# Optimization experiments

Hardware: AMD Instinct MI355X
Metric: run time of the kernel (lower is better)

Reference implementation:

```python
import jax, jax.numpy as jnp
import numpy as np

N_RAYS = 8192
M = 524288
GX, GY, GZ = 160, 160, 128
NFEAT = 12
POS_PE, VIEW_PE = 10, 4
WIDTH = 128
POS_DIM = 3 + 3 * POS_PE * 2      # 63
VIEW_DIM = 3 + 3 * VIEW_PE * 2    # 27
DIM0 = NFEAT + POS_DIM            # 75
ACT_SHIFT = float(np.log(1.0 / (1.0 - 1e-6) - 1.0))  # density bias shift from alpha_init
INTERVAL = 0.5                    # stepsize * voxel_size_ratio
XYZ_MIN, XYZ_MAX = -1.0, 1.0


def posemb(x, n_pe):
    # x: [N,3] -> [N, 3 + 3*n_pe*2], matching cat([x, sin(x*freq), cos(x*freq)])
    freq = 2.0 ** jnp.arange(n_pe, dtype=x.dtype)
    xf = (x[..., None] * freq).reshape(x.shape[0], -1)
    return jnp.concatenate([x, jnp.sin(xf), jnp.cos(xf)], axis=-1)


def trilinear(grid, xyz):
    # grid: [X,Y,Z,C]; xyz: [M,3] in world coords. align_corners=True bilinear (grid_sample).
    sz_f = jnp.array(grid.shape[:3], jnp.float32)
    sz_i = jnp.array(grid.shape[:3], jnp.int32)
    t = (xyz - XYZ_MIN) / (XYZ_MAX - XYZ_MIN) * (sz_f - 1.0)
    t = jnp.clip(t, 0.0, sz_f - 1.0)
    i0 = jnp.clip(jnp.floor(t).astype(jnp.int32), 0, sz_i - 2)
    f = t - i0.astype(t.dtype)
    out = jnp.zeros((xyz.shape[0], grid.shape[-1]), t.dtype)
    for dx in (0, 1):
        for dy in (0, 1):
            for dz in (0, 1):
                w = ((f[:, 0] if dx else 1.0 - f[:, 0])
                     * (f[:, 1] if dy else 1.0 - f[:, 1])
                     * (f[:, 2] if dz else 1.0 - f[:, 2]))
                out = out + w[:, None] * grid[i0[:, 0] + dx, i0[:, 1] + dy, i0[:, 2] + dz]
    return out


def mask_lookup(mask, xyz):
    # nearest-neighbor maskcache_lookup: ijk = round(xyz*scale + shift)
    sz_f = jnp.array(mask.shape, jnp.float32)
    scale = (sz_f - 1.0) / (XYZ_MAX - XYZ_MIN)
    shift = -XYZ_MIN * scale
    ijk = jnp.clip(jnp.round(xyz * scale + shift).astype(jnp.int32), 0,
                   jnp.array(mask.shape, jnp.int32) - 1)
    return mask[ijk[:, 0], ijk[:, 1], ijk[:, 2]]


def alphas2weights(alpha, ray_id, n_rays):
    # segmented T_i = prod_{j<i in ray}(1-alpha_j); weights = T*alpha (ray_id sorted)
    log1a = jnp.log(jnp.clip(1.0 - alpha, 1e-10, 1.0))
    excl = jnp.cumsum(log1a) - log1a                      # global exclusive cumsum
    seg_tot = jax.ops.segment_sum(log1a, ray_id, num_segments=n_rays)
    seg_start = jnp.cumsum(seg_tot) - seg_tot             # exclusive prefix over rays
    T = jnp.exp(excl - seg_start[ray_id])
    weights = T * alpha
    alphainv_last = jnp.exp(seg_tot)
    return weights, alphainv_last


def setup_inputs() -> dict:
    key = jax.random.key(0)
    ks = jax.random.split(key, 16)
    xyz = jax.random.uniform(ks[0], (M, 3), jnp.float32) * (XYZ_MAX - XYZ_MIN) + XYZ_MIN
    ray_id = jnp.sort(jax.random.randint(ks[1], (M,), 0, N_RAYS))
    viewdirs = jax.random.normal(ks[2], (N_RAYS, 3), jnp.float32)
    viewdirs = viewdirs / jnp.linalg.norm(viewdirs, axis=-1, keepdims=True)
    mask = jax.random.uniform(ks[3], (GX, GY, GZ)) > 0.1
    density = jax.random.normal(ks[4], (GX, GY, GZ), jnp.float32) * 0.5
    k0 = jax.random.normal(ks[5], (GX, GY, GZ, NFEAT), jnp.float32) * 0.1
    s = 0.05
    W0 = jax.random.normal(ks[6], (DIM0, WIDTH), jnp.float32) * s
    b0 = jnp.zeros((WIDTH,), jnp.float32)
    W1 = jax.random.normal(ks[7], (WIDTH, WIDTH), jnp.float32) * s
    b1 = jnp.zeros((WIDTH,), jnp.float32)
    W2 = jax.random.normal(ks[8], (WIDTH, WIDTH), jnp.float32) * s
    b2 = jnp.zeros((WIDTH,), jnp.float32)
    Wr = jax.random.normal(ks[9], (WIDTH + VIEW_DIM, 3), jnp.float32) * s
    br = jnp.zeros((3,), jnp.float32)
    return {"xyz": xyz, "ray_id": ray_id, "viewdirs": viewdirs, "mask": mask,
            "density": density, "k0": k0, "W0": W0, "b0": b0, "W1": W1, "b1": b1,
            "W2": W2, "b2": b2, "Wr": Wr, "br": br}


def reference(xyz, ray_id, viewdirs, mask, density, k0, W0, b0, W1, b1, W2, b2, Wr, br):
    # 1) empty-space skipping via mask cache (kept as multiplicative mask for static shapes)
    m = mask_lookup(mask, xyz).astype(xyz.dtype)
    # 2) trilinear density query + raw2alpha
    d = trilinear(density[..., None], xyz)[:, 0]
    alpha = 1.0 - (1.0 + jnp.exp(d + ACT_SHIFT)) ** (-INTERVAL)
    alpha = alpha * m
    # 3) segmented alpha compositing (Alphas2Weights)
    weights, alphainv_last = alphas2weights(alpha, ray_id, N_RAYS)
    # 4) feature query + view MLP -> rgb
    feat = trilinear(k0, xyz)                              # [M, NFEAT]
    h = jnp.concatenate([feat, posemb(xyz, POS_PE)], -1)   # [M, DIM0]
    h = jax.nn.relu(h @ W0 + b0)
    h = jax.nn.relu(h @ W1 + b1)
    h = jax.nn.relu(h @ W2 + b2)
    ve = posemb(viewdirs, VIEW_PE)[ray_id]                 # [M, VIEW_DIM]
    rgb = jax.nn.sigmoid(jnp.concatenate([h, ve], -1) @ Wr + br)
    # 5) composite per ray + white background
    rgb_marched = jax.ops.segment_sum(weights[:, None] * rgb, ray_id, num_segments=N_RAYS)
    rgb_marched = rgb_marched + alphainv_last[:, None] * 1.0
    return rgb_marched
```

## Files before the change

### kernel.cpp

```cpp
#include <hip/hip_runtime.h>
#include <hip/hip_bf16.h>

#define M_SAMPLES 524288
#define NRAYS 8192
#define GXD 160
#define GYD 160
#define GZD 128
#define GYZ (GYD*GZD)
#define NVOX (GXD*GYD*GZD)
#define ACT_SHIFT -13.81550955796f
#define ROWA 136
#define ROWB 136
#define SAMP 64

typedef __bf16 bf16x8 __attribute__((ext_vector_type(8)));
typedef float f32x4 __attribute__((ext_vector_type(4)));
typedef float f32x16 __attribute__((ext_vector_type(16)));
typedef float f32v2 __attribute__((ext_vector_type(2)));

static __device__ inline unsigned short f2bf(float f){
  __hip_bfloat16 h = __float2bfloat16(f);
  unsigned short u; __builtin_memcpy(&u, &h, 2); return u;
}
static __device__ inline float flo(unsigned int u){ return __uint_as_float(u << 16); }
static __device__ inline float fhi(unsigned int u){ return __uint_as_float(u & 0xffff0000u); }

#if defined(__has_builtin)
#if __has_builtin(__builtin_amdgcn_cvt_pk_bf16_f32)
#define HAVE_PK_BF16 1
#endif
#if __has_builtin(__builtin_amdgcn_cvt_pk_f32_fp8) && __has_builtin(__builtin_amdgcn_cvt_pk_fp8_f32)
#define HAVE_FP8 1
#endif
#endif

static __device__ inline unsigned int packbf(float a, float b){
#ifdef HAVE_PK_BF16
  typedef __bf16 bf16v2 __attribute__((ext_vector_type(2)));
  bf16v2 r = __builtin_amdgcn_cvt_pk_bf16_f32(a, b);
  unsigned int u; __builtin_memcpy(&u, &r, 4); return u;
#else
  return (unsigned int)f2bf(a) | ((unsigned int)f2bf(b) << 16);
#endif
}

struct Tri {
  int ix, iy, iz;
  float wx0, wx1, wy0, wy1, wz0, wz1;
};
static __device__ inline Tri tri_setup(float x, float y, float z){
  Tri t;
  float tx = (x+1.f)*0.5f*(float)(GXD-1); tx = fminf(fmaxf(tx,0.f),(float)(GXD-1));
  float ty = (y+1.f)*0.5f*(float)(GYD-1); ty = fminf(fmaxf(ty,0.f),(float)(GYD-1));
  float tz = (z+1.f)*0.5f*(float)(GZD-1); tz = fminf(fmaxf(tz,0.f),(float)(GZD-1));
  t.ix = min((int)tx, GXD-2); t.iy = min((int)ty, GYD-2); t.iz = min((int)tz, GZD-2);
  float fx = tx-t.ix, fy = ty-t.iy, fz = tz-t.iz;
  t.wx0 = 1.f-fx; t.wx1 = fx; t.wy0 = 1.f-fy; t.wy1 = fy; t.wz0 = 1.f-fz; t.wz1 = fz;
  return t;
}

#define NB_REPACK (NVOX/256)
#define NB_W      184
#define NB_RT     (NRAYS/256)
__global__ __launch_bounds__(256) void k_prep(
    const float* __restrict__ density, const float* __restrict__ k0,
    uint4* __restrict__ packed,
    const unsigned int* __restrict__ mw, int* __restrict__ flag,
    const float* __restrict__ W0, const float* __restrict__ W1,
    const float* __restrict__ W2, const float* __restrict__ Wr,
    const float* __restrict__ br,
    unsigned short* __restrict__ wt0, unsigned short* __restrict__ wt1,
    unsigned short* __restrict__ wt2, unsigned short* __restrict__ wtr,
    const float* __restrict__ vd, float* __restrict__ rayterm3)
{
  int b = blockIdx.x;
  if(b < NB_REPACK){
    int v = b*256 + threadIdx.x;
    const float4* kp = (const float4*)(k0 + (size_t)v*12);
    float4 a = kp[0], bb = kp[1], c = kp[2];
#ifdef HAVE_FP8
    uint4 o;
    o.x = __float_as_uint(density[v]);
    int w;
    w = __builtin_amdgcn_cvt_pk_fp8_f32(a.x, a.y, 0, false);
    w = __builtin_amdgcn_cvt_pk_fp8_f32(a.z, a.w, w, true);
    o.y = (unsigned int)w;
    w = __builtin_amdgcn_cvt_pk_fp8_f32(bb.x, bb.y, 0, false);
    w = __builtin_amdgcn_cvt_pk_fp8_f32(bb.z, bb.w, w, true);
    o.z = (unsigned int)w;
    w = __builtin_amdgcn_cvt_pk_fp8_f32(c.x, c.y, 0, false);
    w = __builtin_amdgcn_cvt_pk_fp8_f32(c.z, c.w, w, true);
    o.w = (unsigned int)w;
    packed[v] = o;
#else
    uint4 o0, o1;
    o0.x = __float_as_uint(density[v]);
    o0.y = packbf(a.x, a.y); o0.z = packbf(a.z, a.w); o0.w = packbf(bb.x, bb.y);
    o1.x = packbf(bb.z, bb.w); o1.y = packbf(c.x, c.y); o1.z = packbf(c.z, c.w);
    o1.w = 0;
    packed[(size_t)v*2]   = o0;
    packed[(size_t)v*2+1] = o1;
#endif
    return;
  }
  if(b == NB_REPACK){
    unsigned int v = mw[threadIdx.x & 63];
    unsigned long long any = __ballot(v > 1u);
    if(threadIdx.x == 0) *flag = (any != 0ull) ? 1 : 0;
    return;
  }
  if(b < NB_REPACK + 1 + NB_W){
    int t = (b - NB_REPACK - 1)*256 + threadIdx.x;
    if(t < 128*96){
      int n = t/96, k = t%96;
      wt0[t] = f2bf((k < 75) ? W0[k*128 + n] : 0.f);
    } else if(t < 128*96 + 16384){
      int j = t - 128*96; int n = j/128, k = j%128;
      wt1[j] = f2bf(W1[k*128 + n]);
    } else if(t < 128*96 + 32768){
      int j = t - 128*96 - 16384; int n = j/128, k = j%128;
      wt2[j] = f2bf(W2[k*128 + n]);
    } else if(t < 128*96 + 32768 + 16*128){
      int j = t - 128*96 - 32768; int n = j/128, k = j%128;
      wtr[j] = f2bf((n < 3) ? Wr[k*3 + n] : 0.f);
    }
    return;
  }
  int ray = (b - NB_REPACK - 1 - NB_W)*256 + threadIdx.x;
  if(ray >= NRAYS) return;
  float v0 = vd[ray*3+0], v1 = vd[ray*3+1], v2 = vd[ray*3+2];
  float vej[27];
  vej[0] = v0; vej[1] = v1; vej[2] = v2;
  #pragma unroll
  for(int ci = 0; ci < 3; ++ci){
    float xv = (ci == 0) ? v0 : ((ci == 1) ? v1 : v2);
    #pragma unroll
    for(int p = 0; p < 4; ++p){
      float arg = xv * (float)(1 << p);
      vej[3 + ci*4 + p]  = __sinf(arg);
      vej[15 + ci*4 + p] = __cosf(arg);
    }
  }
  float rt0 = br[0], rt1 = br[1], rt2 = br[2];
  #pragma unroll
  for(int j = 0; j < 27; ++j){
    const float* wr = Wr + (128 + j)*3;
    rt0 += vej[j]*wr[0]; rt1 += vej[j]*wr[1]; rt2 += vej[j]*wr[2];
  }
  rayterm3[ray*3+0] = rt0; rayterm3[ray*3+1] = rt1; rayterm3[ray*3+2] = rt2;
}

template<int KDIM, int SROW, int DROW>
static __device__ inline void layer32(const unsigned short* src, unsigned short* dst,
    const unsigned short* __restrict__ wt, const float* __restrict__ bias,
    int tile_n, int ln, int kh)
{
  constexpr int NS = KDIM/16;
  const unsigned short* wbase  = wt + (tile_n*32 + ln)*KDIM + kh*8;
  const unsigned short* abase0 = src + (ln)*SROW + kh*8;
  const unsigned short* abase1 = src + (32 + ln)*SROW + kh*8;
  f32x16 acc0 = {0.f,0.f,0.f,0.f,0.f,0.f,0.f,0.f,0.f,0.f,0.f,0.f,0.f,0.f,0.f,0.f};
  f32x16 acc1 = acc0;
  __builtin_amdgcn_s_setprio(1);
  #pragma unroll
  for(int st = 0; st < NS; ++st){
    bf16x8 wf = *(const bf16x8*)(wbase + st*16);
    bf16x8 a0 = *(const bf16x8*)(abase0 + st*16);
    bf16x8 a1 = *(const bf16x8*)(abase1 + st*16);
    acc0 = __builtin_amdgcn_mfma_f32_32x32x16_bf16(wf, a0, acc0, 0, 0, 0);
    acc1 = __builtin_amdgcn_mfma_f32_32x32x16_bf16(wf, a1, acc1, 0, 0, 0);
  }
  __builtin_amdgcn_s_setprio(0);
  #pragma unroll
  for(int rep = 0; rep < 2; ++rep){
    const f32x16& acc = rep ? acc1 : acc0;
    int scol = rep*32 + ln;
    #pragma unroll
    for(int g = 0; g < 4; ++g){
      int n0 = tile_n*32 + g*8 + kh*4;
      float4 bv = *(const float4*)(bias + n0);
      unsigned int lo = packbf(fmaxf(acc[4*g+0] + bv.x, 0.f), fmaxf(acc[4*g+1] + bv.y, 0.f));
      unsigned int hi = packbf(fmaxf(acc[4*g+2] + bv.z, 0.f), fmaxf(acc[4*g+3] + bv.w, 0.f));
      unsigned long long o = (unsigned long long)lo | ((unsigned long long)hi << 32);
      *(unsigned long long*)(dst + scol*DROW + n0) = o;
    }
  }
}

template<int PACKED>
__global__ __launch_bounds__(256) void k_mlp(const float* __restrict__ xyz,
    const uint4* __restrict__ packed,
    const float* __restrict__ density, const float* __restrict__ k0,
    const void* __restrict__ mask, const int* __restrict__ flag,
    const int* __restrict__ ray_id,
    const unsigned short* __restrict__ wt0, const unsigned short* __restrict__ wt1,
    const unsigned short* __restrict__ wt2, const unsigned short* __restrict__ wtr,
    const float* __restrict__ b0, const float* __restrict__ b1,
    const float* __restrict__ b2,
    const float* __restrict__ rayterm3, float4* __restrict__ rgba_out)
{
  __shared__ alignas(16) unsigned short hA[SAMP*ROWA];
  __shared__ alignas(16) unsigned short hB[SAMP*ROWB];
  __shared__ float red[SAMP][4];
  __shared__ int ray_s[SAMP];

  int tid = threadIdx.x;
  int lane = tid & 63, wave = tid >> 6;
  int blk = blockIdx.x*SAMP;

  {
    int smp = tid >> 2, corner = tid & 3;
    int i = blk + smp;
    float x = xyz[3*i+0], y = xyz[3*i+1], z = xyz[3*i+2];
    Tri t = tri_setup(x, y, z);
    int dx = corner & 1, dy = corner >> 1;
    float wxy = (dx ? t.wx1 : t.wx0) * (dy ? t.wy1 : t.wy0);
    float w0 = wxy*t.wz0, w1 = wxy*t.wz1;
    size_t vox = (size_t)((t.ix+dx)*GYZ + (t.iy+dy)*GZD + t.iz);
    float pd;
    float pf[12];
#ifdef HAVE_FP8
    if(PACKED){
      uint4 q0 = packed[vox], q1 = packed[vox+1];
      pd = w0*__uint_as_float(q0.x) + w1*__uint_as_float(q1.x);
      f32v2 a, b;
      a = __builtin_amdgcn_cvt_pk_f32_fp8((int)q0.y, false);
      b = __builtin_amdgcn_cvt_pk_f32_fp8((int)q1.y, false);
      pf[0] = w0*a.x + w1*b.x;  pf[1] = w0*a.y + w1*b.y;
      a = __builtin_amdgcn_cvt_pk_f32_fp8((int)q0.y, true);
      b = __builtin_amdgcn_cvt_pk_f32_fp8((int)q1.y, true);
      pf[2] = w0*a.x + w1*b.x;  pf[3] = w0*a.y + w1*b.y;
      a = __builtin_amdgcn_cvt_pk_f32_fp8((int)q0.z, false);
      b = __builtin_amdgcn_cvt_pk_f32_fp8((int)q1.z, false);
      pf[4] = w0*a.x + w1*b.x;  pf[5] = w0*a.y + w1*b.y;
      a = __builtin_amdgcn_cvt_pk_f32_fp8((int)q0.z, true);
      b = __builtin_amdgcn_cvt_pk_f32_fp8((int)q1.z, true);
      pf[6] = w0*a.x + w1*b.x;  pf[7] = w0*a.y + w1*b.y;
      a = __builtin_amdgcn_cvt_pk_f32_fp8((int)q0.w, false);
      b = __builtin_amdgcn_cvt_pk_f32_fp8((int)q1.w, false);
      pf[8] = w0*a.x + w1*b.x;  pf[9] = w0*a.y + w1*b.y;
      a = __builtin_amdgcn_cvt_pk_f32_fp8((int)q0.w, true);
      b = __builtin_amdgcn_cvt_pk_f32_fp8((int)q1.w, true);
      pf[10]= w0*a.x + w1*b.x;  pf[11]= w0*a.y + w1*b.y;
    }
#else
    if(PACKED){
      const uint4* pv = packed + vox*2;
      uint4 q0 = pv[0], q1 = pv[1], q2 = pv[2], q3 = pv[3];
      pd = w0*__uint_as_float(q0.x) + w1*__uint_as_float(q2.x);
      pf[0]  = w0*flo(q0.y) + w1*flo(q2.y);  pf[1]  = w0*fhi(q0.y) + w1*fhi(q2.y);
      pf[2]  = w0*flo(q0.z) + w1*flo(q2.z);  pf[3]  = w0*fhi(q0.z) + w1*fhi(q2.z);
      pf[4]  = w0*flo(q0.w) + w1*flo(q2.w);  pf[5]  = w0*fhi(q0.w) + w1*fhi(q2.w);
      pf[6]  = w0*flo(q1.x) + w1*flo(q3.x);  pf[7]  = w0*fhi(q1.x) + w1*fhi(q3.x);
      pf[8]  = w0*flo(q1.y) + w1*flo(q3.y);  pf[9]  = w0*fhi(q1.y) + w1*fhi(q3.y);
      pf[10] = w0*flo(q1.z) + w1*flo(q3.z);  pf[11] = w0*fhi(q1.z) + w1*fhi(q3.z);
    }
#endif
    if(!PACKED){
      pd = w0*density[vox] + w1*density[vox+1];
      const float4* v = (const float4*)(k0 + vox*12);
      float4 a0 = v[0], a1 = v[1], a2 = v[2];
      float4 c0 = v[3], c1 = v[4], c2 = v[5];
      pf[0] = w0*a0.x + w1*c0.x;  pf[1] = w0*a0.y + w1*c0.y;
      pf[2] = w0*a0.z + w1*c0.z;  pf[3] = w0*a0.w + w1*c0.w;
      pf[4] = w0*a1.x + w1*c1.x;  pf[5] = w0*a1.y + w1*c1.y;
      pf[6] = w0*a1.z + w1*c1.z;  pf[7] = w0*a1.w + w1*c1.w;
      pf[8] = w0*a2.x + w1*c2.x;  pf[9] = w0*a2.y + w1*c2.y;
      pf[10]= w0*a2.z + w1*c2.z;  pf[11]= w0*a2.w + w1*c2.w;
    }
    #pragma unroll
    for(int m2 = 1; m2 < 4; m2 <<= 1){
      pd += __shfl_xor(pd, m2);
      #pragma unroll
      for(int j = 0; j < 12; ++j) pf[j] += __shfl_xor(pf[j], m2);
    }
    if(corner == 0){
      int mx = (int)rintf(x*79.5f + 79.5f); mx = min(max(mx,0), GXD-1);
      int my = (int)rintf(y*79.5f + 79.5f); my = min(max(my,0), GYD-1);
      int mz = (int)rintf(z*63.5f + 63.5f); mz = min(max(mz,0), GZD-1);
      int midx = mx*GYZ + my*GZD + mz;
      bool mm = (*flag) ? (((const unsigned char*)mask)[midx] != 0)
                        : (((const int*)mask)[midx] != 0);
      float e = __expf(pd + ACT_SHIFT);
      float alpha = 1.f - rsqrtf(1.f + e);
      if(!mm) alpha = 0.f;
      red[smp][3] = alpha;
      unsigned int d[8];
      #pragma unroll
      for(int j = 0; j < 6; ++j) d[j] = packbf(pf[2*j], pf[2*j+1]);
      d[6] = packbf(x, y);
      d[7] = packbf(z, __sinf(x));
      uint4* p = (uint4*)(hA + smp*ROWA);
      p[0] = make_uint4(d[0],d[1],d[2],d[3]);
      p[1] = make_uint4(d[4],d[5],d[6],d[7]);
    } else if(corner == 1){
      uint4* p = (uint4*)(hA + smp*ROWA + 80);
      p[0] = make_uint4(0,0,0,0);
      p[1] = make_uint4(0,0,0,0);
      ray_s[smp] = ray_id[i];
    }
  }

  {
    int smp = tid & 63, chunk = 1 + (tid >> 6);
    int i2 = blk + smp;
    float x = xyz[3*i2+0], y = xyz[3*i2+1], z = xyz[3*i2+2];
    float vv[16];
    #pragma unroll
    for(int j = 0; j < 16; ++j){
      int c = chunk*16 + j;
      float r;
      if(c >= 75) r = 0.f;
      else {
        int q = (c < 45) ? (c-15) : (c-45);
        int ci = q/10, p = q - ci*10;
        float xv = (ci == 0) ? x : ((ci == 1) ? y : z);
        float a = xv * (float)(1 << p);
        r = (c < 45) ? __sinf(a) : __cosf(a);
      }
      vv[j] = r;
    }
    unsigned int d[8];
    #pragma unroll
    for(int j = 0; j < 8; ++j) d[j] = packbf(vv[2*j], vv[2*j+1]);
    uint4* p = (uint4*)(hA + smp*ROWA + chunk*16);
    p[0] = make_uint4(d[0],d[1],d[2],d[3]);
    p[1] = make_uint4(d[4],d[5],d[6],d[7]);
  }
  __syncthreads();

  int ln = lane & 31, kh = lane >> 5;
  layer32< 96, ROWA, ROWB>(hA, hB, wt0, b0, wave, ln, kh);  __syncthreads();
  layer32<128, ROWB, ROWA>(hB, hA, wt1, b1, wave, ln, kh);  __syncthreads();
  layer32<128, ROWA, ROWB>(hA, hB, wt2, b2, wave, ln, kh);  __syncthreads();

  {
    int col = lane & 15, q = lane >> 4;
    int mt = wave;
    f32x4 acc = {0.f, 0.f, 0.f, 0.f};
    const unsigned short* arow = hB + (mt*16 + col)*ROWB + q*8;
    const unsigned short* wrow = wtr + col*128 + q*8;
    __builtin_amdgcn_s_setprio(1);
    #pragma unroll
    for(int ks = 0; ks < 4; ++ks){
      bf16x8 af = *(const bf16x8*)(arow + ks*32);
      bf16x8 bfr = *(const bf16x8*)(wrow + ks*32);
      acc = __builtin_amdgcn_mfma_f32_16x16x32_bf16(af, bfr, acc, 0, 0, 0);
    }
    __builtin_amdgcn_s_setprio(0);
    if(col < 3){
      #pragma unroll
      for(int r = 0; r < 4; ++r){
        int sl = mt*16 + q*4 + r;
        float v = acc[r] + rayterm3[ray_s[sl]*3 + col];
        red[sl][col] = __fdividef(1.f, 1.f + __expf(-v));
      }
    }
  }
  __syncthreads();

  if(tid < SAMP){
    rgba_out[blk + tid] = make_float4(red[tid][0], red[tid][1], red[tid][2], red[tid][3]);
  }
}

__global__ __launch_bounds__(256) void k_comp2(const int* __restrict__ ray_id,
    const float4* __restrict__ rgba, float* __restrict__ out)
{
  int r = blockIdx.x*4 + (threadIdx.x >> 6);
  int lane = threadIdx.x & 63;
  int lo = 0, hi = M_SAMPLES;
  while(lo < hi){ int mid = (lo+hi) >> 1; if(ray_id[mid] < r) lo = mid+1; else hi = mid; }
  int s = lo;
  int lo2 = s, hi2 = M_SAMPLES;
  while(lo2 < hi2){ int mid = (lo2+hi2) >> 1; if(ray_id[mid] < r+1) lo2 = mid+1; else hi2 = mid; }
  int e = lo2;

  float carry = 1.f;
  float ar = 0.f, ag = 0.f, ab = 0.f;
  for(int base = s; base < e; base += 64){
    int idx = base + lane;
    float4 c = (idx < e) ? rgba[idx] : make_float4(0.f,0.f,0.f,0.f);
    float a = c.w;
    float incl = 1.f - a;
    #pragma unroll
    for(int d2 = 1; d2 < 64; d2 <<= 1){
      float t = __shfl_up(incl, d2);
      if(lane >= d2) incl *= t;
    }
    float excl = __shfl_up(incl, 1);
    if(lane == 0) excl = 1.f;
    float w = carry * excl * a;
    ar += w*c.x; ag += w*c.y; ab += w*c.z;
    carry *= __shfl(incl, 63);
  }
  #pragma unroll
  for(int m2 = 1; m2 < 64; m2 <<= 1){
    ar += __shfl_xor(ar, m2);
    ag += __shfl_xor(ag, m2);
    ab += __shfl_xor(ab, m2);
  }
  if(lane == 0){
    out[3*r+0] = ar + carry;
    out[3*r+1] = ag + carry;
    out[3*r+2] = ab + carry;
  }
}

extern "C" void kernel_launch(void* const* d_in, const int* in_sizes, int n_in,
                              void* d_out, int out_size, void* d_ws, size_t ws_size,
                              hipStream_t stream)
{
  const float* xyz      = (const float*)d_in[0];
  const int*   ray_id   = (const int*)  d_in[1];
  const float* viewdirs = (const float*)d_in[2];
  const void*  mask     =               d_in[3];
  const float* density  = (const float*)d_in[4];
  const float* k0       = (const float*)d_in[5];
  const float* W0 = (const float*)d_in[6];  const float* b0 = (const float*)d_in[7];
  const float* W1 = (const float*)d_in[8];  const float* b1 = (const float*)d_in[9];
  const float* W2 = (const float*)d_in[10]; const float* b2 = (const float*)d_in[11];
  const float* Wr = (const float*)d_in[12]; const float* br = (const float*)d_in[13];
  float* out = (float*)d_out;

  char* ws = (char*)d_ws;
  size_t off = 0;
  auto take = [&](size_t nbytes) -> void* {
    void* p = ws + off;
    off = (off + nbytes + 255) & ~(size_t)255;
    return p;
  };
  int*            flag     = (int*)           take(4);
  unsigned short* wt0      = (unsigned short*)take(128*96*2);
  unsigned short* wt1      = (unsigned short*)take(128*128*2);
  unsigned short* wt2      = (unsigned short*)take(128*128*2);
  unsigned short* wtr      = (unsigned short*)take(16*128*2);
  float*          rayterm3 = (float*)         take((size_t)NRAYS*3*4);
  float4*         rgba_ws  = (float4*)        take((size_t)M_SAMPLES*16);
#ifdef HAVE_FP8
  uint4*          packed   = (uint4*)         take((size_t)NVOX*16);
#else
  uint4*          packed   = (uint4*)         take((size_t)NVOX*32);
#endif
  bool use_packed = (ws_size >= off);

  k_prep<<<NB_REPACK + 1 + NB_W + NB_RT, 256, 0, stream>>>(
      density, k0, packed, (const unsigned int*)mask, flag,
      W0, W1, W2, Wr, br, wt0, wt1, wt2, wtr, viewdirs, rayterm3);
  if(use_packed){
    k_mlp<1><<<M_SAMPLES/SAMP, 256, 0, stream>>>(xyz, packed, density, k0, mask, flag,
                                                 ray_id, wt0, wt1, wt2, wtr,
                                                 b0, b1, b2, rayterm3, rgba_ws);
  } else {
    k_mlp<0><<<M_SAMPLES/SAMP, 256, 0, stream>>>(xyz, packed, density, k0, mask, flag,
                                                 ray_id, wt0, wt1, wt2, wtr,
                                                 b0, b1, b2, rayterm3, rgba_ws);
  }
  k_comp2<<<NRAYS/4, 256, 0, stream>>>(ray_id, rgba_ws, out);
}
```

Measured before the change: 422.2 us.

## Prefetch next-layer MLP weights into registers during current layer epilogue

Splits the per-layer MFMA routine into compute, weight-load and epilogue parts so each layer's global weight fragments are loaded into registers before they are needed. The first layer's weights load before the trilinear gather, and later weights and the head weights are fetched while the previous layer's epilogue runs. Launch bounds also gain a minimum-blocks hint of 4. This hides global weight-load latency behind other work, at the cost of more live registers and possible spills under the occupancy constraint.

Result: no change. 417.1 us (-1.2%).

```diff
diff --git a/kernel.cpp b/kernel.cpp
--- a/kernel.cpp
+++ b/kernel.cpp
@@ -150,27 +150,39 @@
   rayterm3[ray*3+0] = rt0; rayterm3[ray*3+1] = rt1; rayterm3[ray*3+2] = rt2;
 }
 
-template<int KDIM, int SROW, int DROW>
-static __device__ inline void layer32(const unsigned short* src, unsigned short* dst,
-    const unsigned short* __restrict__ wt, const float* __restrict__ bias,
-    int tile_n, int ln, int kh)
+template<int KDIM, int SROW>
+static __device__ __forceinline__ void mfma_layer(const unsigned short* src,
+    const bf16x8* wf, f32x16& acc0, f32x16& acc1, int ln, int kh)
 {
   constexpr int NS = KDIM/16;
-  const unsigned short* wbase  = wt + (tile_n*32 + ln)*KDIM + kh*8;
   const unsigned short* abase0 = src + (ln)*SROW + kh*8;
   const unsigned short* abase1 = src + (32 + ln)*SROW + kh*8;
-  f32x16 acc0 = {0.f,0.f,0.f,0.f,0.f,0.f,0.f,0.f,0.f,0.f,0.f,0.f,0.f,0.f,0.f,0.f};
-  f32x16 acc1 = acc0;
+  f32x16 z = {0.f,0.f,0.f,0.f,0.f,0.f,0.f,0.f,0.f,0.f,0.f,0.f,0.f,0.f,0.f,0.f};
+  acc0 = z; acc1 = z;
   __builtin_amdgcn_s_setprio(1);
   #pragma unroll
   for(int st = 0; st < NS; ++st){
-    bf16x8 wf = *(const bf16x8*)(wbase + st*16);
     bf16x8 a0 = *(const bf16x8*)(abase0 + st*16);
     bf16x8 a1 = *(const bf16x8*)(abase1 + st*16);
-    acc0 = __builtin_amdgcn_mfma_f32_32x32x16_bf16(wf, a0, acc0, 0, 0, 0);
-    acc1 = __builtin_amdgcn_mfma_f32_32x32x16_bf16(wf, a1, acc1, 0, 0, 0);
+    acc0 = __builtin_amdgcn_mfma_f32_32x32x16_bf16(wf[st], a0, acc0, 0, 0, 0);
+    acc1 = __builtin_amdgcn_mfma_f32_32x32x16_bf16(wf[st], a1, acc1, 0, 0, 0);
   }
   __builtin_amdgcn_s_setprio(0);
+}
+
+template<int NS>
+static __device__ __forceinline__ void load_wf(const unsigned short* wbase, bf16x8* wf){
+  #pragma unroll
+  for(int st = 0; st < NS; ++st) wf[st] = *(const bf16x8*)(wbase + st*16);
+}
+
+template<int DROW>
+static __device__ __forceinline__ void epilogue(const f32x16& acc0, const f32x16& acc1,
+    unsigned short* dst, const float* __restrict__ bias, int tile_n, int ln, int kh)
+{
+  float4 bv[4];
+  #pragma unroll
+  for(int g = 0; g < 4; ++g) bv[g] = *(const float4*)(bias + tile_n*32 + g*8 + kh*4);
   #pragma unroll
   for(int rep = 0; rep < 2; ++rep){
     const f32x16& acc = rep ? acc1 : acc0;
@@ -178,9 +190,8 @@
     #pragma unroll
     for(int g = 0; g < 4; ++g){
       int n0 = tile_n*32 + g*8 + kh*4;
-      float4 bv = *(const float4*)(bias + n0);
-      unsigned int lo = packbf(fmaxf(acc[4*g+0] + bv.x, 0.f), fmaxf(acc[4*g+1] + bv.y, 0.f));
-      unsigned int hi = packbf(fmaxf(acc[4*g+2] + bv.z, 0.f), fmaxf(acc[4*g+3] + bv.w, 0.f));
+      unsigned int lo = packbf(fmaxf(acc[4*g+0] + bv[g].x, 0.f), fmaxf(acc[4*g+1] + bv[g].y, 0.f));
+      unsigned int hi = packbf(fmaxf(acc[4*g+2] + bv[g].z, 0.f), fmaxf(acc[4*g+3] + bv[g].w, 0.f));
       unsigned long long o = (unsigned long long)lo | ((unsigned long long)hi << 32);
       *(unsigned long long*)(dst + scol*DROW + n0) = o;
     }
@@ -188,7 +199,7 @@
 }
 
 template<int PACKED>
-__global__ __launch_bounds__(256) void k_mlp(const float* __restrict__ xyz,
+__global__ __launch_bounds__(256, 4) void k_mlp(const float* __restrict__ xyz,
     const uint4* __restrict__ packed,
     const float* __restrict__ density, const float* __restrict__ k0,
     const void* __restrict__ mask, const int* __restrict__ flag,
@@ -207,6 +218,10 @@
   int tid = threadIdx.x;
   int lane = tid & 63, wave = tid >> 6;
   int blk = blockIdx.x*SAMP;
+  int ln = lane & 31, kh = lane >> 5;
+
+  bf16x8 wf[8];
+  load_wf<6>(wt0 + (wave*32 + ln)*96 + kh*8, wf);
 
   {
     int smp = tid >> 2, corner = tid & 3;
@@ -329,29 +344,44 @@
   }
   __syncthreads();
 
-  int ln = lane & 31, kh = lane >> 5;
-  layer32< 96, ROWA, ROWB>(hA, hB, wt0, b0, wave, ln, kh);  __syncthreads();
-  layer32<128, ROWB, ROWA>(hB, hA, wt1, b1, wave, ln, kh);  __syncthreads();
-  layer32<128, ROWA, ROWB>(hA, hB, wt2, b2, wave, ln, kh);  __syncthreads();
-
+  f32x16 acc0, acc1;
+
+  mfma_layer<96, ROWA>(hA, wf, acc0, acc1, ln, kh);
+  load_wf<8>(wt1 + (wave*32 + ln)*128 + kh*8, wf);
+  epilogue<ROWB>(acc0, acc1, hB, b0, wave, ln, kh);
+  __syncthreads();
+
+  mfma_layer<128, ROWB>(hB, wf, acc0, acc1, ln, kh);
+  load_wf<8>(wt2 + (wave*32 + ln)*128 + kh*8, wf);
+  epilogue<ROWA>(acc0, acc1, hA, b1, wave, ln, kh);
+  __syncthreads();
+
+  int col = lane & 15, q4 = lane >> 4;
+  mfma_layer<128, ROWA>(hA, wf, acc0, acc1, ln, kh);
+  bf16x8 hw[4];
   {
-    int col = lane & 15, q = lane >> 4;
+    const unsigned short* wr = wtr + col*128 + q4*8;
+    #pragma unroll
+    for(int ks = 0; ks < 4; ++ks) hw[ks] = *(const bf16x8*)(wr + ks*32);
+  }
+  epilogue<ROWB>(acc0, acc1, hB, b2, wave, ln, kh);
+  __syncthreads();
+
+  {
     int mt = wave;
     f32x4 acc = {0.f, 0.f, 0.f, 0.f};
-    const unsigned short* arow = hB + (mt*16 + col)*ROWB + q*8;
-    const unsigned short* wrow = wtr + col*128 + q*8;
+    const unsigned short* arow = hB + (mt*16 + col)*ROWB + q4*8;
     __builtin_amdgcn_s_setprio(1);
     #pragma unroll
     for(int ks = 0; ks < 4; ++ks){
       bf16x8 af = *(const bf16x8*)(arow + ks*32);
-      bf16x8 bfr = *(const bf16x8*)(wrow + ks*32);
-      acc = __builtin_amdgcn_mfma_f32_16x16x32_bf16(af, bfr, acc, 0, 0, 0);
+      acc = __builtin_amdgcn_mfma_f32_16x16x32_bf16(af, hw[ks], acc, 0, 0, 0);
     }
     __builtin_amdgcn_s_setprio(0);
     if(col < 3){
       #pragma unroll
       for(int r = 0; r < 4; ++r){
-        int sl = mt*16 + q*4 + r;
+        int sl = mt*16 + q4*4 + r;
         float v = acc[r] + rayterm3[ray_s[sl]*3 + col];
         red[sl][col] = __fdividef(1.f, 1.f + __expf(-v));
       }
```
